# Optimization experiments

Measured on AMD Instinct MI355X. Metric: run time of the kernel, lower is better.

## Reference

```python
import jax, jax.numpy as jnp
import numpy as np

C_IN = 256
RED = 8
C_QK = C_IN // RED  # 32


def setup_inputs() -> dict:
    key = jax.random.key(0)
    ks = jax.random.split(key, 8)
    B, C, H, W = 4, C_IN, 64, 64
    x = jax.random.normal(ks[0], (B, C, H, W), dtype=jnp.float32)
    # 1x1 conv weights stored as (out_ch, in_ch); biases (out_ch,)
    s = 1.0 / np.sqrt(C)
    wq = jax.random.uniform(ks[1], (C_QK, C), minval=-s, maxval=s, dtype=jnp.float32)
    bq = jax.random.uniform(ks[2], (C_QK,), minval=-s, maxval=s, dtype=jnp.float32)
    wk = jax.random.uniform(ks[3], (C_QK, C), minval=-s, maxval=s, dtype=jnp.float32)
    bk = jax.random.uniform(ks[4], (C_QK,), minval=-s, maxval=s, dtype=jnp.float32)
    wv = jax.random.uniform(ks[5], (C, C), minval=-s, maxval=s, dtype=jnp.float32)
    bv = jax.random.uniform(ks[6], (C,), minval=-s, maxval=s, dtype=jnp.float32)
    # nn.Parameter(torch.zeros(1)) -> use small nonzero so gradients flow in tests
    gamma = jnp.full((1,), 0.5, dtype=jnp.float32)
    return {"x": x, "wq": wq, "bq": bq, "wk": wk, "bk": bk,
            "wv": wv, "bv": bv, "gamma": gamma}


def reference(x, wq, bq, wk, bk, wv, bv, gamma):
    B, C, H, W = x.shape
    N = H * W
    xf = x.reshape(B, C, N)                                  # (B,C,N)
    # 1x1 convs == per-pixel linear projections over channels
    q = jnp.einsum('dc,bcn->bdn', wq, xf) + bq[None, :, None]  # (B,Cqk,N)
    k = jnp.einsum('dc,bcn->bdn', wk, xf) + bk[None, :, None]  # (B,Cqk,N)
    v = jnp.einsum('oc,bcn->bon', wv, xf) + bv[None, :, None]  # (B,C,N)
    # attention[b,i,j] = <q[:,i], k[:,j]> ; softmax over j (no scaling, as in source)
    scores = jnp.einsum('bdi,bdj->bij', q, k)                 # (B,N,N)
    attn = jax.nn.softmax(scores, axis=-1)
    # out[b,c,i] = sum_j v[b,c,j] * attn[b,i,j]
    out = jnp.einsum('bcj,bij->bci', v, attn).reshape(B, C, H, W)
    return gamma * out + x
```

## Files before the change

### kernel.cpp

```cpp
#include <hip/hip_runtime.h>
#include <hip/hip_bf16.h>


#define NB     4
#define CC     256
#define CQK    32
#define NPIX   4096
#define NCHUNK 4
#define CHUNK  (NPIX / NCHUNK)
#define NT     (CHUNK / 64)

typedef float floatx4 __attribute__((ext_vector_type(4)));
typedef short shortx4 __attribute__((ext_vector_type(4)));
typedef short shortx8 __attribute__((ext_vector_type(8)));

__device__ __forceinline__ short f2bf(float f) {
  unsigned u = __float_as_uint(f);
  u += 0x7fffu + ((u >> 16) & 1u);
  return (short)(u >> 16);
}
__device__ __forceinline__ float bf2f(unsigned short u) {
  return __uint_as_float((unsigned)u << 16);
}
__device__ __forceinline__ unsigned pk2bf(float a, float b) {
  union { __hip_bfloat162 h; unsigned u; } cv;
  cv.h = __float22bfloat162_rn(make_float2(a, b));
  return cv.u;
}
__device__ __forceinline__ void gload16(const void* g, void* l) {
  __builtin_amdgcn_global_load_lds(
      (const __attribute__((address_space(1))) void*)g,
      (__attribute__((address_space(3))) void*)l, 16, 0, 0);
}

__global__ __launch_bounds__(256) void prep_kernel(
    const float* __restrict__ wq, const float* __restrict__ wk,
    const float* __restrict__ wv, short* __restrict__ Wall)
{
  const int e = (blockIdx.x * 256 + threadIdx.x) * 4;
  const int o = e >> 8, c = e & 255;
  const float* src = (o < 32) ? (wq + (size_t)o * CC + c)
                   : (o < 64) ? (wk + (size_t)(o - 32) * CC + c)
                              : (wv + (size_t)(o - 64) * CC + c);
  const floatx4 v = *(const floatx4*)src;
  shortx4 r;
#pragma unroll
  for (int i = 0; i < 4; i++) r[i] = f2bf(v[i]);
  *(shortx4*)(Wall + e) = r;
}

__global__ __launch_bounds__(256) void xt_kernel(
    const float* __restrict__ x, short* __restrict__ xT)
{
  __shared__ short T[64][72];
  const int gid = blockIdx.x;
  const int b = gid >> 8, r = gid & 255;
  const int c0 = (r >> 6) * 64, n0 = (r & 63) * 64;
  const int t = threadIdx.x;

  const int cl = t >> 2, nq = (t & 3) * 16;
  const float* src = x + ((size_t)(b * CC + c0 + cl)) * NPIX + n0 + nq;
  floatx4 v[4];
#pragma unroll
  for (int q = 0; q < 4; q++) v[q] = *(const floatx4*)(src + q * 4);
#pragma unroll
  for (int i = 0; i < 16; i++) {
    const int n = nq + i;
    const int csw = cl ^ ((i & 7) << 3);
    T[n][csw] = f2bf(v[i >> 2][i & 3]);
  }
  __syncthreads();

  const int nl = t >> 2, cq = (t & 3) * 16;
  const int X = (nl & 7) << 3;
  const shortx8 g0 = *(const shortx8*)&T[nl][(cq) ^ X];
  const shortx8 g1 = *(const shortx8*)&T[nl][(cq + 8) ^ X];
  short* dst = xT + ((size_t)(b * NPIX + n0 + nl)) * CC + c0 + cq;
  *(shortx8*)dst = g0;
  *(shortx8*)(dst + 8) = g1;
}

__global__ __launch_bounds__(256) void proj_kernel(
    const short* __restrict__ Wall,
    const float* __restrict__ bq, const float* __restrict__ bk,
    const float* __restrict__ bv,
    const short* __restrict__ xT,
    short* __restrict__ Qb, short* __restrict__ Kb, short* __restrict__ Vb)
{
  const int gid = blockIdx.x;
  const int b = gid / 320, r2 = gid % 320;
  const int og = r2 >> 6, nt = r2 & 63, n0 = nt * 64;
  const int tid = threadIdx.x, lane = tid & 63, w = tid >> 6;
  const int lo = lane & 15, hi = lane >> 4;

  const short* arow = Wall + (size_t)(og * 64 + w * 16 + lo) * CC + hi * 8;
  const short* brow = xT + ((size_t)(b * NPIX + n0 + lo)) * CC + hi * 8;

  floatx4 acc[4];
#pragma unroll
  for (int ct = 0; ct < 4; ct++) acc[ct] = (floatx4){0.f, 0.f, 0.f, 0.f};

#pragma unroll
  for (int c0 = 0; c0 < CC; c0 += 32) {
    const shortx8 a = *(const shortx8*)(arow + c0);
#pragma unroll
    for (int ct = 0; ct < 4; ct++) {
      const shortx8 bf = *(const shortx8*)(brow + (size_t)ct * 16 * CC + c0);
      acc[ct] = __builtin_amdgcn_mfma_f32_16x16x32_bf16(a, bf, acc[ct], 0, 0, 0);
    }
  }

#pragma unroll
  for (int j = 0; j < 4; j++) {
    const int o = og * 64 + w * 16 + hi * 4 + j;
    const float bias = (o < 32) ? bq[o] : (o < 64) ? bk[o - 32] : bv[o - 64];
#pragma unroll
    for (int ct = 0; ct < 4; ct++) {
      const int n = n0 + ct * 16 + lo;
      float val = acc[ct][j] + bias;
      if (o < 32) val *= 1.44269504088896f;
      const short v = f2bf(val);
      if (o < 32)       Qb[((size_t)(b * NPIX + n)) * CQK + o] = v;
      else if (o < 64)  Kb[((size_t)(b * NPIX + n)) * CQK + (o - 32)] = v;
      else              Vb[((size_t)(b * CC + (o - 64))) * NPIX + n] = v;
    }
  }
}

__global__ __launch_bounds__(256, 2) void attn_kernel(
    const short* __restrict__ Qb, const short* __restrict__ Kb,
    const short* __restrict__ Vb,
    short* __restrict__ Opart, float* __restrict__ Lpart)
{
  __shared__ short Vl[2][16384];
  __shared__ short Kl[2][2048];
  __shared__ short Pl[4][1024];

  const int bc = blockIdx.x & 15, qt = blockIdx.x >> 4;
  const int b = bc & 3, ch = bc >> 2;
  const int q0 = qt * 128, kv0 = ch * CHUNK;
  const int tid = threadIdx.x, lane = tid & 63, w = tid >> 6;
  const int lo = lane & 15, hi = lane >> 4;

  const short* Kc = Kb + ((size_t)(b * NPIX + kv0)) * CQK;
  const short* Vc = Vb + (size_t)b * CC * NPIX + kv0;

  shortx8 qf[2];
#pragma unroll
  for (int qs = 0; qs < 2; qs++)
    qf[qs] = *(const shortx8*)(
        Qb + ((size_t)(b * NPIX + q0 + w * 32 + qs * 16 + lo)) * CQK + hi * 8);

  const int cV = w * 64 + (lane >> 3);
  const int pcV = lane & 7;
  const int kvK = w * 16 + (lane >> 2);
  const int lcK = (lane & 3) ^ ((kvK >> 1) & 3);

  floatx4 oacc[2][16];
#pragma unroll
  for (int qs = 0; qs < 2; qs++)
#pragma unroll
    for (int i = 0; i < 16; i++) oacc[qs][i] = (floatx4){0.f, 0.f, 0.f, 0.f};
  float l[2] = {0.f, 0.f};
  const floatx4 zero4 = (floatx4){0.f, 0.f, 0.f, 0.f};

#pragma unroll
  for (int i = 0; i < 8; i++) {
    const int c = cV + i * 8;
    gload16(Vc + (size_t)c * NPIX + (pcV ^ (c & 7)) * 8, &Vl[0][w * 4096 + i * 512]);
  }
  gload16(Kc + (size_t)kvK * CQK + lcK * 8, &Kl[0][w * 512]);
  __syncthreads();

  for (int t = 0; t < NT; t++) {
    const int buf = t & 1;

    if (t + 1 < NT) {
      const int j0n = (t + 1) * 64;
#pragma unroll
      for (int i = 0; i < 8; i++) {
        const int c = cV + i * 8;
        gload16(Vc + (size_t)c * NPIX + j0n + (pcV ^ (c & 7)) * 8,
                &Vl[buf ^ 1][w * 4096 + i * 512]);
      }
      gload16(Kc + (size_t)(j0n + kvK) * CQK + lcK * 8, &Kl[buf ^ 1][w * 512]);
    }

    floatx4 s[2][4];
#pragma unroll
    for (int ct = 0; ct < 4; ct++) {
      const int kv = ct * 16 + lo;
      const shortx8 kf = *(const shortx8*)
          &Kl[buf][kv * 32 + ((hi * 8) ^ (((kv >> 1) & 3) << 3))];
      s[0][ct] = __builtin_amdgcn_mfma_f32_16x16x32_bf16(kf, qf[0], zero4, 0, 0, 0);
      s[1][ct] = __builtin_amdgcn_mfma_f32_16x16x32_bf16(kf, qf[1], zero4, 0, 0, 0);
    }

    shortx8 pb[2][2];
#pragma unroll
    for (int qs = 0; qs < 2; qs++) {
      float rs = 0.f;
#pragma unroll
      for (int ct = 0; ct < 4; ct++) {
        const float p0 = exp2f(s[qs][ct][0]), p1 = exp2f(s[qs][ct][1]);
        const float p2 = exp2f(s[qs][ct][2]), p3 = exp2f(s[qs][ct][3]);
        rs += (p0 + p1) + (p2 + p3);
        uint2 u;
        u.x = pk2bf(p0, p1);
        u.y = pk2bf(p2, p3);
        *(uint2*)&Pl[w][lo * 64 + ((ct * 16 + hi * 4) ^ ((lo & 7) << 3))] = u;
      }
#pragma unroll
      for (int h = 0; h < 2; h++)
        pb[qs][h] = *(const shortx8*)
            &Pl[w][lo * 64 + ((h * 32 + hi * 8) ^ ((lo & 7) << 3))];
      rs += __shfl_xor(rs, 16);
      rs += __shfl_xor(rs, 32);
      l[qs] += rs;
    }

#pragma unroll
    for (int ctv = 0; ctv < 16; ctv++) {
      const int c = ctv * 16 + lo;
      const int swz = (c & 7) << 3;
      const shortx8 va0 = *(const shortx8*)&Vl[buf][c * 64 + ((hi * 8) ^ swz)];
      const shortx8 va1 = *(const shortx8*)&Vl[buf][c * 64 + ((32 + hi * 8) ^ swz)];
      oacc[0][ctv] = __builtin_amdgcn_mfma_f32_16x16x32_bf16(va0, pb[0][0], oacc[0][ctv], 0, 0, 0);
      oacc[0][ctv] = __builtin_amdgcn_mfma_f32_16x16x32_bf16(va1, pb[0][1], oacc[0][ctv], 0, 0, 0);
      oacc[1][ctv] = __builtin_amdgcn_mfma_f32_16x16x32_bf16(va0, pb[1][0], oacc[1][ctv], 0, 0, 0);
      oacc[1][ctv] = __builtin_amdgcn_mfma_f32_16x16x32_bf16(va1, pb[1][1], oacc[1][ctv], 0, 0, 0);
    }

    __syncthreads();
  }

  if (hi == 0) {
    Lpart[(size_t)bc * NPIX + q0 + w * 32 + lo] = l[0];
    Lpart[(size_t)bc * NPIX + q0 + w * 32 + 16 + lo] = l[1];
  }
#pragma unroll
  for (int qs = 0; qs < 2; qs++) {
    const int n = q0 + w * 32 + qs * 16 + lo;
#pragma unroll
    for (int ctv = 0; ctv < 16; ctv++)
#pragma unroll
      for (int j = 0; j < 4; j++) {
        const int c = ctv * 16 + hi * 4 + j;
        Opart[((size_t)bc * CC + c) * NPIX + n] = f2bf(oacc[qs][ctv][j]);
      }
  }
}

__global__ __launch_bounds__(256) void combine_kernel(
    const short* __restrict__ Opart, const float* __restrict__ Lpart,
    const float* __restrict__ x, const float* __restrict__ gamma,
    float* __restrict__ out)
{
  __shared__ float linv[512];
  const int gid = blockIdx.x;
  const int b = gid >> 7;
  const int c0 = ((gid >> 3) & 15) * 16;
  const int n0 = (gid & 7) * 512;
  const int t = threadIdx.x;

  if (t < 128) {
    const int n = n0 + t * 4;
    floatx4 sum = (floatx4){0.f, 0.f, 0.f, 0.f};
#pragma unroll
    for (int k = 0; k < NCHUNK; k++)
      sum += *(const floatx4*)(Lpart + (size_t)(k * NB + b) * NPIX + n);
#pragma unroll
    for (int i = 0; i < 4; i++) linv[t * 4 + i] = 1.0f / sum[i];
  }
  __syncthreads();

  const float g = gamma[0];
  const int il = t & 63, cw = t >> 6;
  const int n = n0 + il * 8;
  float li[8];
#pragma unroll
  for (int j = 0; j < 8; j++) li[j] = linv[il * 8 + j];

#pragma unroll
  for (int i = 0; i < 4; i++) {
    const int c = c0 + cw * 4 + i;
    float acc[8];
#pragma unroll
    for (int j = 0; j < 8; j++) acc[j] = 0.f;
#pragma unroll
    for (int k = 0; k < NCHUNK; k++) {
      const shortx8 o = *(const shortx8*)(
          Opart + ((size_t)((k * NB + b) * CC + c)) * NPIX + n);
#pragma unroll
      for (int j = 0; j < 8; j++) acc[j] += bf2f((unsigned short)o[j]);
    }
    const size_t idx = ((size_t)(b * CC + c)) * NPIX + n;
    const floatx4 x0 = *(const floatx4*)(x + idx);
    const floatx4 x1 = *(const floatx4*)(x + idx + 4);
    floatx4 r0, r1;
#pragma unroll
    for (int j = 0; j < 4; j++) {
      r0[j] = g * (acc[j] * li[j]) + x0[j];
      r1[j] = g * (acc[j + 4] * li[j + 4]) + x1[j];
    }
    *(floatx4*)(out + idx) = r0;
    *(floatx4*)(out + idx + 4) = r1;
  }
}

extern "C" void kernel_launch(void* const* d_in, const int* in_sizes, int n_in,
                              void* d_out, int out_size, void* d_ws, size_t ws_size,
                              hipStream_t stream) {
  const float* x     = (const float*)d_in[0];
  const float* wq    = (const float*)d_in[1];
  const float* bq    = (const float*)d_in[2];
  const float* wk    = (const float*)d_in[3];
  const float* bk    = (const float*)d_in[4];
  const float* wv    = (const float*)d_in[5];
  const float* bv    = (const float*)d_in[6];
  const float* gamma = (const float*)d_in[7];
  float* out = (float*)d_out;

  char* p = (char*)d_ws;
  short* Wall  = (short*)p; p += (size_t)320 * CC * 2;
  short* xT    = (short*)p; p += (size_t)NB * NPIX * CC * 2;
  short* Qb    = (short*)p; p += (size_t)NB * NPIX * CQK * 2;
  short* Kb    = (short*)p; p += (size_t)NB * NPIX * CQK * 2;
  short* Vb    = (short*)p; p += (size_t)NB * CC * NPIX * 2;
  short* Opart = (short*)p; p += (size_t)(NCHUNK * NB) * CC * NPIX * 2;
  float* Lpart = (float*)p; p += (size_t)(NCHUNK * NB) * NPIX * 4;

  prep_kernel<<<dim3(80), dim3(256), 0, stream>>>(wq, wk, wv, Wall);
  xt_kernel<<<dim3(1024), dim3(256), 0, stream>>>(x, xT);
  proj_kernel<<<dim3(1280), dim3(256), 0, stream>>>(Wall, bq, bk, bv, xT, Qb, Kb, Vb);
  attn_kernel<<<dim3(512), dim3(256), 0, stream>>>(Qb, Kb, Vb, Opart, Lpart);
  combine_kernel<<<dim3(512), dim3(256), 0, stream>>>(Opart, Lpart, x, gamma, out);
}
```

Measured before the change: 167.3 us.

## Fuse weight conversion, x transpose and QKV projection into one kernel

Replaces the three kernels (weight bf16 conversion, x transpose, projection) with a single kernel. Each block loads and transposes a 64-pixel tile of x for all 256 channels into shared memory, converts fp32 weights to bf16 on the fly, computes all 320 output rows with MFMA, and stages outputs through LDS for coalesced Q/K/V stores. This removes two launches and the global round trip of the xT and Wall buffers. In exchange it uses a large shared-memory tile, runs only 256 blocks, and converts the weights redundantly in every block.

After: 161.2 us. 1.04x faster.

```diff
diff --git a/kernel.cpp b/kernel.cpp
--- a/kernel.cpp
+++ b/kernel.cpp
@@ -33,96 +33,117 @@
       (__attribute__((address_space(3))) void*)l, 16, 0, 0);
 }
 
-__global__ __launch_bounds__(256) void prep_kernel(
-    const float* __restrict__ wq, const float* __restrict__ wk,
-    const float* __restrict__ wv, short* __restrict__ Wall)
-{
-  const int e = (blockIdx.x * 256 + threadIdx.x) * 4;
-  const int o = e >> 8, c = e & 255;
-  const float* src = (o < 32) ? (wq + (size_t)o * CC + c)
-                   : (o < 64) ? (wk + (size_t)(o - 32) * CC + c)
-                              : (wv + (size_t)(o - 64) * CC + c);
-  const floatx4 v = *(const floatx4*)src;
-  shortx4 r;
-#pragma unroll
-  for (int i = 0; i < 4; i++) r[i] = f2bf(v[i]);
-  *(shortx4*)(Wall + e) = r;
-}
-
-__global__ __launch_bounds__(256) void xt_kernel(
-    const float* __restrict__ x, short* __restrict__ xT)
-{
-  __shared__ short T[64][72];
-  const int gid = blockIdx.x;
-  const int b = gid >> 8, r = gid & 255;
-  const int c0 = (r >> 6) * 64, n0 = (r & 63) * 64;
-  const int t = threadIdx.x;
-
-  const int cl = t >> 2, nq = (t & 3) * 16;
-  const float* src = x + ((size_t)(b * CC + c0 + cl)) * NPIX + n0 + nq;
-  floatx4 v[4];
-#pragma unroll
-  for (int q = 0; q < 4; q++) v[q] = *(const floatx4*)(src + q * 4);
-#pragma unroll
-  for (int i = 0; i < 16; i++) {
-    const int n = nq + i;
-    const int csw = cl ^ ((i & 7) << 3);
-    T[n][csw] = f2bf(v[i >> 2][i & 3]);
-  }
-  __syncthreads();
-
-  const int nl = t >> 2, cq = (t & 3) * 16;
-  const int X = (nl & 7) << 3;
-  const shortx8 g0 = *(const shortx8*)&T[nl][(cq) ^ X];
-  const shortx8 g1 = *(const shortx8*)&T[nl][(cq + 8) ^ X];
-  short* dst = xT + ((size_t)(b * NPIX + n0 + nl)) * CC + c0 + cq;
-  *(shortx8*)dst = g0;
-  *(shortx8*)(dst + 8) = g1;
-}
-
-__global__ __launch_bounds__(256) void proj_kernel(
-    const short* __restrict__ Wall,
-    const float* __restrict__ bq, const float* __restrict__ bk,
-    const float* __restrict__ bv,
-    const short* __restrict__ xT,
+__global__ __launch_bounds__(256) void projx_kernel(
+    const float* __restrict__ x,
+    const float* __restrict__ wq, const float* __restrict__ bq,
+    const float* __restrict__ wk, const float* __restrict__ bk,
+    const float* __restrict__ wv, const float* __restrict__ bv,
     short* __restrict__ Qb, short* __restrict__ Kb, short* __restrict__ Vb)
 {
+  __shared__ short U[256 * 72 + 64 * 72];
+
   const int gid = blockIdx.x;
-  const int b = gid / 320, r2 = gid % 320;
-  const int og = r2 >> 6, nt = r2 & 63, n0 = nt * 64;
-  const int tid = threadIdx.x, lane = tid & 63, w = tid >> 6;
+  const int b = gid >> 6, n0 = (gid & 63) * 64;
+  const int t = threadIdx.x, lane = t & 63, w = t >> 6;
   const int lo = lane & 15, hi = lane >> 4;
 
-  const short* arow = Wall + (size_t)(og * 64 + w * 16 + lo) * CC + hi * 8;
-  const short* brow = xT + ((size_t)(b * NPIX + n0 + lo)) * CC + hi * 8;
-
-  floatx4 acc[4];
-#pragma unroll
-  for (int ct = 0; ct < 4; ct++) acc[ct] = (floatx4){0.f, 0.f, 0.f, 0.f};
+  {
+    const int cl = t >> 2;
+    const int nq = (t & 3) * 16;
+#pragma unroll
+    for (int rr = 0; rr < 4; rr++) {
+      const float* src = x + ((size_t)(b * CC + rr * 64 + cl)) * NPIX + n0 + nq;
+      floatx4 v[4];
+#pragma unroll
+      for (int q = 0; q < 4; q++) v[q] = *(const floatx4*)(src + q * 4);
+#pragma unroll
+      for (int i = 0; i < 16; i++) {
+        const int n = nq + i;
+        U[n * 256 + rr * 64 + (cl ^ ((i & 7) << 3))] = f2bf(v[i >> 2][i & 3]);
+      }
+    }
+  }
+  __syncthreads();
+
+  const float* wrow[5];
+#pragma unroll
+  for (int rt = 0; rt < 5; rt++) {
+    const int o = w * 80 + rt * 16 + lo;
+    wrow[rt] = (o < 32) ? (wq + (size_t)o * CC)
+             : (o < 64) ? (wk + (size_t)(o - 32) * CC)
+                        : (wv + (size_t)(o - 64) * CC);
+  }
+
+  floatx4 acc[5][4];
+#pragma unroll
+  for (int r = 0; r < 5; r++)
+#pragma unroll
+    for (int c = 0; c < 4; c++) acc[r][c] = (floatx4){0.f, 0.f, 0.f, 0.f};
 
 #pragma unroll
   for (int c0 = 0; c0 < CC; c0 += 32) {
-    const shortx8 a = *(const shortx8*)(arow + c0);
+    shortx8 bf[4];
 #pragma unroll
     for (int ct = 0; ct < 4; ct++) {
-      const shortx8 bf = *(const shortx8*)(brow + (size_t)ct * 16 * CC + c0);
-      acc[ct] = __builtin_amdgcn_mfma_f32_16x16x32_bf16(a, bf, acc[ct], 0, 0, 0);
-    }
-  }
-
-#pragma unroll
-  for (int j = 0; j < 4; j++) {
-    const int o = og * 64 + w * 16 + hi * 4 + j;
-    const float bias = (o < 32) ? bq[o] : (o < 64) ? bk[o - 32] : bv[o - 64];
-#pragma unroll
-    for (int ct = 0; ct < 4; ct++) {
-      const int n = n0 + ct * 16 + lo;
-      float val = acc[ct][j] + bias;
-      if (o < 32) val *= 1.44269504088896f;
-      const short v = f2bf(val);
-      if (o < 32)       Qb[((size_t)(b * NPIX + n)) * CQK + o] = v;
-      else if (o < 64)  Kb[((size_t)(b * NPIX + n)) * CQK + (o - 32)] = v;
-      else              Vb[((size_t)(b * CC + (o - 64))) * NPIX + n] = v;
+      const int n = ct * 16 + lo;
+      const int c = c0 + hi * 8;
+      bf[ct] = *(const shortx8*)
+          &U[n * 256 + (c & 192) + ((c & 63) ^ ((n & 7) << 3))];
+    }
+#pragma unroll
+    for (int rt = 0; rt < 5; rt++) {
+      const float* ap = wrow[rt] + c0 + hi * 8;
+      floatx4 a0 = *(const floatx4*)ap;
+      floatx4 a1 = *(const floatx4*)(ap + 4);
+      if (w == 0 && rt < 2) {
+        a0 *= 1.44269504088896f; a1 *= 1.44269504088896f;
+      }
+      union { shortx8 s; unsigned u[4]; } au;
+      au.u[0] = pk2bf(a0[0], a0[1]);
+      au.u[1] = pk2bf(a0[2], a0[3]);
+      au.u[2] = pk2bf(a1[0], a1[1]);
+      au.u[3] = pk2bf(a1[2], a1[3]);
+#pragma unroll
+      for (int ct = 0; ct < 4; ct++)
+        acc[rt][ct] = __builtin_amdgcn_mfma_f32_16x16x32_bf16(au.s, bf[ct], acc[rt][ct], 0, 0, 0);
+    }
+  }
+
+  __syncthreads();
+
+#pragma unroll
+  for (int rt = 0; rt < 5; rt++) {
+#pragma unroll
+    for (int j = 0; j < 4; j++) {
+      const int o = w * 80 + rt * 16 + hi * 4 + j;
+      const float bs = (o < 32) ? bq[o] * 1.44269504088896f
+                     : (o < 64) ? bk[o - 32] : bv[o - 64];
+#pragma unroll
+      for (int ct = 0; ct < 4; ct++) {
+        const int n = ct * 16 + lo;
+        const short hv = f2bf(acc[rt][ct][j] + bs);
+        if (o < 64) U[256 * 72 + n * 72 + o] = hv;
+        else        U[(o - 64) * 72 + n] = hv;
+      }
+    }
+  }
+  __syncthreads();
+
+#pragma unroll
+  for (int it = 0; it < 8; it++) {
+    const int ov = it * 32 + (t >> 3);
+    const int seg = (t & 7) * 8;
+    const shortx8 d = *(const shortx8*)&U[ov * 72 + seg];
+    *(shortx8*)(Vb + ((size_t)(b * CC + ov)) * NPIX + n0 + seg) = d;
+  }
+  if (w < 2) {
+    const int n = lane;
+    short* dst = (w == 0 ? Qb : Kb) + ((size_t)(b * NPIX + n0 + n)) * CQK;
+    const int off = 256 * 72 + n * 72 + w * 32;
+#pragma unroll
+    for (int s = 0; s < 4; s++) {
+      const shortx8 d = *(const shortx8*)&U[off + s * 8];
+      *(shortx8*)(dst + s * 8) = d;
     }
   }
 }
@@ -322,17 +343,13 @@
   float* out = (float*)d_out;
 
   char* p = (char*)d_ws;
-  short* Wall  = (short*)p; p += (size_t)320 * CC * 2;
-  short* xT    = (short*)p; p += (size_t)NB * NPIX * CC * 2;
   short* Qb    = (short*)p; p += (size_t)NB * NPIX * CQK * 2;
   short* Kb    = (short*)p; p += (size_t)NB * NPIX * CQK * 2;
   short* Vb    = (short*)p; p += (size_t)NB * CC * NPIX * 2;
   short* Opart = (short*)p; p += (size_t)(NCHUNK * NB) * CC * NPIX * 2;
   float* Lpart = (float*)p; p += (size_t)(NCHUNK * NB) * NPIX * 4;
 
-  prep_kernel<<<dim3(80), dim3(256), 0, stream>>>(wq, wk, wv, Wall);
-  xt_kernel<<<dim3(1024), dim3(256), 0, stream>>>(x, xT);
-  proj_kernel<<<dim3(1280), dim3(256), 0, stream>>>(Wall, bq, bk, bv, xT, Qb, Kb, Vb);
+  projx_kernel<<<dim3(256), dim3(256), 0, stream>>>(x, wq, bq, wk, bk, wv, bv, Qb, Kb, Vb);
   attn_kernel<<<dim3(512), dim3(256), 0, stream>>>(Qb, Kb, Vb, Opart, Lpart);
   combine_kernel<<<dim3(512), dim3(256), 0, stream>>>(Opart, Lpart, x, gamma, out);
 }
```
